# Kernel tuning notes

Measured on AMD Instinct MI355X. Metric: run time of the kernel, lower is better.

## Reference

```python
import jax, jax.numpy as jnp
import numpy as np

OUT_CH = 64
K = 7

def setup_inputs() -> dict:
    key = jax.random.key(0)
    k1, k2 = jax.random.split(key)
    data = jax.random.normal(k1, (32, 1, 224, 224), dtype=jnp.float32)
    # torch Conv2d default init: uniform(-b, b), b = 1/sqrt(in_ch*k*k)
    bound = 1.0 / np.sqrt(1 * K * K)
    weight = jax.random.uniform(k2, (OUT_CH, 1, K, K), dtype=jnp.float32,
                                minval=-bound, maxval=bound)
    return {"data": data, "weight": weight}

def reference(data, weight):
    # Valid (padding=0) stride-1 conv, NCHW x OIHW -> NCHW
    return jax.lax.conv_general_dilated(
        data, weight,
        window_strides=(1, 1),
        padding="VALID",
        dimension_numbers=("NCHW", "OIHW", "NCHW"),
    )
```

## Files before the change

kernel.cpp:

```cpp
#include <hip/hip_runtime.h>
#include <hip/hip_bf16.h>

#define IN_H  224
#define IN_W  224
#define OUT_H 218
#define OUT_W 218
#define NCH   64
#define PLANE (OUT_H * OUT_W)
#define RSH   464
#define CP1   232
#define NROW  4
#define NYB   55
#define NMT   4
#define OCH   876
#define NBLK  (32 * NMT * NYB)

typedef short bf16x8 __attribute__((ext_vector_type(8)));
typedef float f32x4  __attribute__((ext_vector_type(4)));

__device__ inline unsigned int f2bf(float f) {
    unsigned int u = __builtin_bit_cast(unsigned int, f);
    return (u + 0x7fffu + ((u >> 16) & 1u)) >> 16;
}

__device__ inline unsigned int pk2(float lo, float hi) {
    __hip_bfloat162 h2 = __float22bfloat162_rn(make_float2(lo, hi));
    unsigned int u;
    __builtin_memcpy(&u, &h2, sizeof(u));
    return u;
}

__global__ __launch_bounds__(512) void repack_w(const float* __restrict__ wgt,
                                                unsigned int* __restrict__ wa) {
    const int t    = threadIdx.x;
    const int lane = t & 63;
    const int fc   = t >> 6;
    const int mt   = fc >> 1, kt = fc & 1;
    const int ch   = 16 * mt + (lane & 15);
    const int dy   = 4 * kt + (lane >> 4);
    unsigned int w[4];
#pragma unroll
    for (int j = 0; j < 4; ++j) {
        float lo = (dy < 7 && 2 * j     < 7) ? wgt[ch * 49 + dy * 7 + 2 * j]     : 0.f;
        float hi = (dy < 7 && 2 * j + 1 < 7) ? wgt[ch * 49 + dy * 7 + 2 * j + 1] : 0.f;
        w[j] = f2bf(lo) | (f2bf(hi) << 16);
    }
    reinterpret_cast<uint4*>(wa)[fc * 64 + lane] = make_uint4(w[0], w[1], w[2], w[3]);
}

__global__ __launch_bounds__(512) void conv7x7_row(
    const float* __restrict__ in,
    const unsigned int* __restrict__ wa,
    float* __restrict__ out)
{
    __shared__ unsigned short tbf[10 * RSH];
    __shared__ float obuf[16 * OCH];

    const int tid  = threadIdx.x;
    const int lane = tid & 63;
    const int wid  = tid >> 6;
    const int g    = lane >> 4;
    const int c    = lane & 15;

    const int bid  = blockIdx.x;
    const int rank = (bid & 7) * (NBLK / 8) + (bid >> 3);
    const int n    = rank / (NMT * NYB);
    const int rem  = rank - n * (NMT * NYB);
    const int mt   = rem / NYB;
    const int yb   = rem - mt * NYB;
    const int y0   = yb * NROW;

    union AB { uint4 u; bf16x8 v; };
    AB af[2];
    const uint4* wa4 = reinterpret_cast<const uint4*>(wa);
#pragma unroll
    for (int kt = 0; kt < 2; ++kt) af[kt].u = wa4[(mt * 2 + kt) * 64 + lane];

    const float* inb = in + (size_t)n * (IN_H * IN_W);
    for (int idx = tid; idx < 10 * 58; idx += 512) {
        int r = idx / 58, c4 = idx - r * 58;
        int iny = min(y0 + r, IN_H - 1);
        const float* rp = inb + iny * IN_W;
        float4 v = (c4 < 56) ? *reinterpret_cast<const float4*>(rp + 4 * c4)
                             : make_float4(0.f, 0.f, 0.f, 0.f);
        float nx = (c4 < 55) ? rp[4 * c4 + 4] : 0.f;
        uint2 w0 = make_uint2(pk2(v.x, v.y), pk2(v.z, v.w));
        uint2 w1 = make_uint2(pk2(v.y, v.z), pk2(v.w, nx));
        *reinterpret_cast<uint2*>(&tbf[r * RSH + 4 * c4])       = w0;
        *reinterpret_cast<uint2*>(&tbf[r * RSH + CP1 + 4 * c4]) = w1;
    }
    __syncthreads();

    const int sh = c & 1;
    for (int k = wid; k < 4 * 14; k += 8) {
        const int r  = k / 14;
        const int x0 = 16 * (k - 14 * r);
        const int e0 = x0 + c - sh;

        AB bf[2];
#pragma unroll
        for (int kt = 0; kt < 2; ++kt) {
            const int row = min(r + 4 * kt + g, 9);
            const unsigned int* p = reinterpret_cast<const unsigned int*>(
                &tbf[row * RSH + sh * CP1 + e0]);
            union { unsigned int u[4]; uint4 q; } bb;
            bb.u[0] = p[0]; bb.u[1] = p[1]; bb.u[2] = p[2]; bb.u[3] = p[3];
            bf[kt].u = bb.q;
        }

        f32x4 acc = {0.f, 0.f, 0.f, 0.f};
        acc = __builtin_amdgcn_mfma_f32_16x16x32_bf16(af[0].v, bf[0].v, acc, 0, 0, 0);
        acc = __builtin_amdgcn_mfma_f32_16x16x32_bf16(af[1].v, bf[1].v, acc, 0, 0, 0);

        if (x0 + c < OUT_W) {
#pragma unroll
            for (int rr = 0; rr < 4; ++rr)
                obuf[(4 * g + rr) * OCH + r * OUT_W + x0 + c] = acc[rr];
        }
    }
    __syncthreads();

    const int vrows = min(NROW, OUT_H - y0);
    const int nf4   = (vrows * OUT_W) >> 2;
    const size_t base = ((size_t)(n * NCH + 16 * mt)) * PLANE + (size_t)y0 * OUT_W;
#pragma unroll
    for (int i = 0; i < 2; ++i) {
        const int p = 2 * wid + i;
        const float* src = &obuf[p * OCH];
        float* dst = out + base + (size_t)p * PLANE;
#pragma unroll
        for (int j = 0; j < 4; ++j) {
            int idx = 64 * j + lane;
            if (idx < nf4) {
                f32x4 v = *reinterpret_cast<const f32x4*>(src + 4 * idx);
                __builtin_nontemporal_store(v, reinterpret_cast<f32x4*>(dst + 4 * idx));
            }
        }
    }
}

extern "C" void kernel_launch(void* const* d_in, const int* in_sizes, int n_in,
                              void* d_out, int out_size, void* d_ws, size_t ws_size,
                              hipStream_t stream) {
    const float* in  = (const float*)d_in[0];
    const float* wgt = (const float*)d_in[1];
    float* out = (float*)d_out;
    unsigned int* wa = (unsigned int*)d_ws;

    repack_w<<<1, 512, 0, stream>>>(wgt, wa);
    conv7x7_row<<<NBLK, 512, 0, stream>>>(in, wa, out);
}
```

Measured before the change: 100.3 us.

## Fuse weight repack into conv kernel and drop nontemporal output stores

```diff
diff --git a/kernel.cpp b/kernel.cpp
--- a/kernel.cpp
+++ b/kernel.cpp
@@ -18,11 +18,6 @@
 typedef short bf16x8 __attribute__((ext_vector_type(8)));
 typedef float f32x4  __attribute__((ext_vector_type(4)));
 
-__device__ inline unsigned int f2bf(float f) {
-    unsigned int u = __builtin_bit_cast(unsigned int, f);
-    return (u + 0x7fffu + ((u >> 16) & 1u)) >> 16;
-}
-
 __device__ inline unsigned int pk2(float lo, float hi) {
     __hip_bfloat162 h2 = __float22bfloat162_rn(make_float2(lo, hi));
     unsigned int u;
@@ -30,27 +25,16 @@
     return u;
 }
 
-__global__ __launch_bounds__(512) void repack_w(const float* __restrict__ wgt,
-                                                unsigned int* __restrict__ wa) {
-    const int t    = threadIdx.x;
-    const int lane = t & 63;
-    const int fc   = t >> 6;
-    const int mt   = fc >> 1, kt = fc & 1;
-    const int ch   = 16 * mt + (lane & 15);
-    const int dy   = 4 * kt + (lane >> 4);
-    unsigned int w[4];
-#pragma unroll
-    for (int j = 0; j < 4; ++j) {
-        float lo = (dy < 7 && 2 * j     < 7) ? wgt[ch * 49 + dy * 7 + 2 * j]     : 0.f;
-        float hi = (dy < 7 && 2 * j + 1 < 7) ? wgt[ch * 49 + dy * 7 + 2 * j + 1] : 0.f;
-        w[j] = f2bf(lo) | (f2bf(hi) << 16);
-    }
-    reinterpret_cast<uint4*>(wa)[fc * 64 + lane] = make_uint4(w[0], w[1], w[2], w[3]);
+__device__ inline void bar_lgkm() {
+    asm volatile("s_waitcnt lgkmcnt(0)" ::: "memory");
+    __builtin_amdgcn_sched_barrier(0);
+    __builtin_amdgcn_s_barrier();
+    __builtin_amdgcn_sched_barrier(0);
 }
 
 __global__ __launch_bounds__(512) void conv7x7_row(
     const float* __restrict__ in,
-    const unsigned int* __restrict__ wa,
+    const float* __restrict__ wgt,
     float* __restrict__ out)
 {
     __shared__ unsigned short tbf[10 * RSH];
@@ -70,11 +54,8 @@
     const int yb   = rem - mt * NYB;
     const int y0   = yb * NROW;
 
-    union AB { uint4 u; bf16x8 v; };
-    AB af[2];
-    const uint4* wa4 = reinterpret_cast<const uint4*>(wa);
-#pragma unroll
-    for (int kt = 0; kt < 2; ++kt) af[kt].u = wa4[(mt * 2 + kt) * 64 + lane];
+    const float* wsrc = wgt + mt * (16 * 49);
+    for (int idx = tid; idx < 784; idx += 512) obuf[idx] = wsrc[idx];
 
     const float* inb = in + (size_t)n * (IN_H * IN_W);
     for (int idx = tid; idx < 10 * 58; idx += 512) {
@@ -88,6 +69,24 @@
         uint2 w1 = make_uint2(pk2(v.y, v.z), pk2(v.w, nx));
         *reinterpret_cast<uint2*>(&tbf[r * RSH + 4 * c4])       = w0;
         *reinterpret_cast<uint2*>(&tbf[r * RSH + CP1 + 4 * c4]) = w1;
+    }
+    __syncthreads();
+
+    union AB { uint4 u; bf16x8 v; };
+    AB af[2];
+    {
+        const int c16 = lane & 15;
+#pragma unroll
+        for (int kt = 0; kt < 2; ++kt) {
+            const int dy = 4 * kt + g;
+            if (dy < 7) {
+                const float* wr = &obuf[c16 * 49 + dy * 7];
+                af[kt].u = make_uint4(pk2(wr[0], wr[1]), pk2(wr[2], wr[3]),
+                                      pk2(wr[4], wr[5]), pk2(wr[6], 0.f));
+            } else {
+                af[kt].u = make_uint4(0u, 0u, 0u, 0u);
+            }
+        }
     }
     __syncthreads();
 
@@ -118,7 +117,7 @@
                 obuf[(4 * g + rr) * OCH + r * OUT_W + x0 + c] = acc[rr];
         }
     }
-    __syncthreads();
+    bar_lgkm();
 
     const int vrows = min(NROW, OUT_H - y0);
     const int nf4   = (vrows * OUT_W) >> 2;
@@ -131,10 +130,9 @@
 #pragma unroll
         for (int j = 0; j < 4; ++j) {
             int idx = 64 * j + lane;
-            if (idx < nf4) {
-                f32x4 v = *reinterpret_cast<const f32x4*>(src + 4 * idx);
-                __builtin_nontemporal_store(v, reinterpret_cast<f32x4*>(dst + 4 * idx));
-            }
+            if (idx < nf4)
+                *reinterpret_cast<float4*>(dst + 4 * idx) =
+                    *reinterpret_cast<const float4*>(src + 4 * idx);
         }
     }
 }
@@ -145,8 +143,6 @@
     const float* in  = (const float*)d_in[0];
     const float* wgt = (const float*)d_in[1];
     float* out = (float*)d_out;
-    unsigned int* wa = (unsigned int*)d_ws;
 
-    repack_w<<<1, 512, 0, stream>>>(wgt, wa);
-    conv7x7_row<<<NBLK, 512, 0, stream>>>(in, wa, out);
+    conv7x7_row<<<NBLK, 512, 0, stream>>>(in, wgt, out);
 }
```

After: 83.46 us. -16.8%, faster.
